# Performance work log

Hardware: AMD Instinct MI355X
Metric: run time of the kernel (lower is better)

## Reference

```python
import jax, jax.numpy as jnp
import numpy as np

B, N, C, K, H, W = 2, 16, 256, 64, 64, 64
NUM_HEADS = 8


def setup_inputs() -> dict:
    key = jax.random.key(0)
    ks = jax.random.split(key, 7)
    return {
        "value": jax.random.normal(ks[0], (B, N, C, H, W), dtype=jnp.float32),
        "key_map": jax.random.normal(ks[1], (B, K, H, W), dtype=jnp.float32),
        "state": jax.random.normal(ks[2], (B, N, K, C), dtype=jnp.float32),
        "b_w": jax.random.normal(ks[3], (NUM_HEADS, C), dtype=jnp.float32) * 0.06,
        "a_w": jax.random.normal(ks[4], (NUM_HEADS, C), dtype=jnp.float32) * 0.06,
        "A_log": jax.random.normal(ks[5], (NUM_HEADS,), dtype=jnp.float32),
        "dt_bias": jax.random.normal(ks[6], (NUM_HEADS,), dtype=jnp.float32),
    }


def reference(value, key_map, state, b_w, a_w, A_log, dt_bias):
    # Gated delta-rule erase-write memory update (state != None branch).
    num_heads = b_w.shape[0]
    rep = value.shape[2] // num_heads  # value_dim // num_heads

    # softmax over key channel dim (stable; matches max-subtract + softmax)
    key_n = jax.nn.softmax(key_map, axis=1)  # [B,K,H,W]

    # v_k = einsum('bkhw, bjhw,bnjv -> bnkv'): fuse via key gram matrix
    # (avoids materializing v_old [B,N,C,H,W])
    gram = jnp.einsum('bkhw,bjhw->bkj', key_n, key_n)      # [B,K,K]
    v_k = jnp.einsum('bkj,bnjv->bnkv', gram, state)        # [B,N,K,C]

    # erase gate beta: sigmoid(state @ b_proj^T), repeat over head groups
    beta = jax.nn.sigmoid(jnp.einsum('bnkc,hc->bnkh', state, b_w))
    beta = jnp.repeat(beta, rep, axis=3)                   # [B,N,K,C]

    # write term
    vk_t = jnp.einsum('bkhw,bnvhw->bnkv', key_n, value)    # [B,N,K,C]

    # decay gate alpha = -exp(A_log) * softplus(state @ a_proj^T + dt_bias)
    alpha = -jnp.exp(A_log) * jax.nn.softplus(
        jnp.einsum('bnkc,hc->bnkh', state, a_w) + dt_bias)
    alpha = jnp.repeat(alpha, rep, axis=3)                 # [B,N,K,C]

    new_state = alpha * (state - beta * v_k) + beta * vk_t  # [B,N,K,C]

    readout = jnp.einsum('bkhw,bnkv->bnvhw', key_n, new_state)  # [B,N,C,H,W]
    return readout
```

## Files before the change

kernel.cpp:

```cpp
#include <hip/hip_runtime.h>
#include <hip/hip_bf16.h>

#define BB 2
#define NN 16
#define CC 256
#define KK 64
#define HW 4096
#define NH 8

typedef __attribute__((ext_vector_type(4))) float f32x4;
typedef __attribute__((ext_vector_type(8))) short s16x8;
typedef __attribute__((ext_vector_type(4))) short s16x4;

__device__ __forceinline__ short f2bf(float f) {
    __hip_bfloat16 h = __float2bfloat16(f);
    return *reinterpret_cast<short*>(&h);
}
__device__ __forceinline__ float bf2f(short s) {
    unsigned int u = ((unsigned int)(unsigned short)s) << 16;
    float f; __builtin_memcpy(&f, &u, 4); return f;
}

__global__ __launch_bounds__(256) void k_pre(const float* __restrict__ state,
                                             const float* __restrict__ b_w,
                                             const float* __restrict__ a_w,
                                             const float* __restrict__ A_log,
                                             const float* __restrict__ dt_bias,
                                             float* __restrict__ betaH,
                                             float* __restrict__ alphaH,
                                             const float* __restrict__ km,
                                             short* __restrict__ kbf,
                                             short* __restrict__ kbfT) {
    __shared__ float red[4][2 * NH];
    const int tid = threadIdx.x;
    const int bid = blockIdx.x;

    if (bid < BB * NN * KK) {
        const int id = bid;
        const int bn = id >> 6;
        const int k = id & 63;
        const float s = state[((size_t)bn * KK + k) * CC + tid];

        float pb[NH], pa[NH];
#pragma unroll
        for (int h = 0; h < NH; h++) {
            pb[h] = s * b_w[h * CC + tid];
            pa[h] = s * a_w[h * CC + tid];
        }
#pragma unroll
        for (int off = 32; off; off >>= 1) {
#pragma unroll
            for (int h = 0; h < NH; h++) {
                pb[h] += __shfl_down(pb[h], off, 64);
                pa[h] += __shfl_down(pa[h], off, 64);
            }
        }
        const int wave = tid >> 6, lane = tid & 63;
        if (lane == 0) {
#pragma unroll
            for (int h = 0; h < NH; h++) { red[wave][h] = pb[h]; red[wave][NH + h] = pa[h]; }
        }
        __syncthreads();
        const int h = tid >> 5;
        float braw = 0.f, araw = 0.f;
#pragma unroll
        for (int w = 0; w < 4; w++) { braw += red[w][h]; araw += red[w][NH + h]; }
        if ((tid & 31) == 0) {
            const float beta = 1.f / (1.f + __expf(-braw));
            const float xx = araw + dt_bias[h];
            const float sp = fmaxf(xx, 0.f) + log1pf(__expf(-fabsf(xx)));
            const float alpha = -__expf(A_log[h]) * sp;
            betaH[(size_t)id * NH + h] = beta;
            alphaH[(size_t)id * NH + h] = alpha;
        }
    } else {
        const int sid = bid - BB * NN * KK;
        const int b = sid >> 5;
        const int w = tid >> 6, lane = tid & 63;
        const int hw = (sid & 31) * 128 + w * 32 + (lane & 31);
        const int half = lane >> 5;
        const float* p = km + ((size_t)b * KK + half * 32) * HW + hw;
        float x[32];
        float m = -1e30f;
#pragma unroll
        for (int k = 0; k < 32; k++) { x[k] = p[(size_t)k * HW]; m = fmaxf(m, x[k]); }
        m = fmaxf(m, __shfl_xor(m, 32, 64));
        float s = 0.f;
#pragma unroll
        for (int k = 0; k < 32; k++) { x[k] = __expf(x[k] - m); s += x[k]; }
        s += __shfl_xor(s, 32, 64);
        const float inv = 1.f / s;
        short* q2 = kbf + ((size_t)b * KK + half * 32) * HW + hw;
#pragma unroll
        for (int k = 0; k < 32; k++) {
            x[k] *= inv;
            q2[(size_t)k * HW] = f2bf(x[k]);
        }
        short* q3 = kbfT + ((size_t)b * HW + hw) * KK + half * 32;
#pragma unroll
        for (int k8 = 0; k8 < 32; k8 += 8) {
            s16x8 v;
#pragma unroll
            for (int j = 0; j < 8; j++) v[j] = f2bf(x[k8 + j]);
            *(s16x8*)(q3 + k8) = v;
        }
    }
}

__global__ __launch_bounds__(256) void k_gram(const short* __restrict__ kbf,
                                              float* __restrict__ gram) {
    const int tid = threadIdx.x;
    const int id = blockIdx.x;
    const int b = (id >= 2080) ? 1 : 0;
    const int t = id - b * 2080;
    int k = (int)((sqrtf(8.f * (float)t + 1.f) - 1.f) * 0.5f);
    while ((k + 1) * (k + 2) / 2 <= t) k++;
    while (k * (k + 1) / 2 > t) k--;
    const int j = t - k * (k + 1) / 2;

    const short* pa = kbf + ((size_t)b * KK + k) * HW + tid * 16;
    const short* pb = kbf + ((size_t)b * KK + j) * HW + tid * 16;
    const s16x8 a0 = *(const s16x8*)pa, a1 = *(const s16x8*)(pa + 8);
    const s16x8 b0 = *(const s16x8*)pb, b1 = *(const s16x8*)(pb + 8);
    float s = 0.f;
#pragma unroll
    for (int i = 0; i < 8; i++) {
        s = fmaf(bf2f(a0[i]), bf2f(b0[i]), s);
        s = fmaf(bf2f(a1[i]), bf2f(b1[i]), s);
    }
#pragma unroll
    for (int off = 32; off; off >>= 1) s += __shfl_down(s, off, 64);
    __shared__ float red[4];
    if ((tid & 63) == 0) red[tid >> 6] = s;
    __syncthreads();
    if (tid == 0) {
        const float tot = red[0] + red[1] + red[2] + red[3];
        gram[((size_t)b * KK + k) * KK + j] = tot;
        gram[((size_t)b * KK + j) * KK + k] = tot;
    }
}

__global__ __launch_bounds__(512) void k_vkt_part(const short* __restrict__ kbf,
                                                  const float* __restrict__ value,
                                                  short* __restrict__ pbuf) {
    const int tid = threadIdx.x;
    const int id = blockIdx.x;
    const int hs = id & 15;
    const int bn = id >> 4;
    const int b  = bn >> 4;
    const int w = tid >> 6, lane = tid & 63;
    const int l15 = lane & 15, hi = lane >> 4;
    const int hw0 = hs * 256;

    __shared__ short Bs[2][256 * 64];
    __shared__ short As[2][64 * 64];

    const int sr = tid >> 3;
    const int sj = tid & 7;
    const float* vbase = value + (size_t)bn * CC * HW + hw0;
    const short* abase = kbf + ((size_t)b * KK + sr) * HW + hw0 + sj * 8;

    f32x4 stgB[2][4][2];
    s16x8 stgA[2];

#define LOADREG(set_, t_)                                                      \
    {                                                                          \
        _Pragma("unroll") for (int i = 0; i < 4; i++) {                        \
            const float* p_ = vbase + (size_t)(sr + i * 64) * HW               \
                              + (t_) * 64 + sj * 8;                            \
            stgB[set_][i][0] = *(const f32x4*)p_;                              \
            stgB[set_][i][1] = *(const f32x4*)(p_ + 4);                        \
        }                                                                      \
        stgA[set_] = *(const s16x8*)(abase + (t_) * 64);                       \
    }
#define WRITE_LDS(set_, buf_)                                                  \
    {                                                                          \
        _Pragma("unroll") for (int i = 0; i < 4; i++) {                        \
            const int r_ = sr + i * 64;                                        \
            s16x8 tv_;                                                         \
            _Pragma("unroll") for (int e = 0; e < 4; e++) {                    \
                tv_[e]     = f2bf(stgB[set_][i][0][e]);                        \
                tv_[4 + e] = f2bf(stgB[set_][i][1][e]);                        \
            }                                                                  \
            *(s16x8*)&Bs[buf_][r_ * 64 + ((sj ^ (r_ & 7)) * 8)] = tv_;         \
        }                                                                      \
        *(s16x8*)&As[buf_][sr * 64 + ((sj ^ (sr & 7)) * 8)] = stgA[set_];      \
    }

    f32x4 acc[2][4];
#pragma unroll
    for (int m2 = 0; m2 < 2; m2++)
#pragma unroll
        for (int n4 = 0; n4 < 4; n4++) acc[m2][n4] = (f32x4){0.f, 0.f, 0.f, 0.f};

    LOADREG(0, 0);
    LOADREG(1, 1);
    WRITE_LDS(0, 0);
    asm volatile("s_waitcnt lgkmcnt(0)" ::: "memory");
    __builtin_amdgcn_s_barrier();

#pragma unroll
    for (int t = 0; t < 4; t++) {
        const int buf = t & 1;
        if (t + 2 < 4) LOADREG(buf, t + 2);
        if (t + 1 < 4) WRITE_LDS((t + 1) & 1, (t + 1) & 1);

        const int swz = l15 & 7;
#pragma unroll
        for (int s = 0; s < 2; s++) {
            s16x8 vfr[2];
#pragma unroll
            for (int m2 = 0; m2 < 2; m2++)
                vfr[m2] = *(const s16x8*)&Bs[buf][(w * 32 + m2 * 16 + l15) * 64 +
                                                 (((s * 4 + hi) ^ swz) * 8)];
#pragma unroll
            for (int n4 = 0; n4 < 4; n4++) {
                const s16x8 afr = *(const s16x8*)&As[buf][(n4 * 16 + l15) * 64 +
                                                          (((s * 4 + hi) ^ swz) * 8)];
                acc[0][n4] = __builtin_amdgcn_mfma_f32_16x16x32_bf16(vfr[0], afr,
                                                                     acc[0][n4], 0, 0, 0);
                acc[1][n4] = __builtin_amdgcn_mfma_f32_16x16x32_bf16(vfr[1], afr,
                                                                     acc[1][n4], 0, 0, 0);
            }
        }
        if (t + 1 < 4) {
            asm volatile("s_waitcnt lgkmcnt(0)" ::: "memory");
            __builtin_amdgcn_s_barrier();
        }
    }
#undef LOADREG
#undef WRITE_LDS

#pragma unroll
    for (int m2 = 0; m2 < 2; m2++)
#pragma unroll
        for (int n4 = 0; n4 < 4; n4++) {
            s16x4 v;
#pragma unroll
            for (int r = 0; r < 4; r++) v[r] = f2bf(acc[m2][n4][r]);
            *(s16x4*)(pbuf + ((((size_t)(id * 8 + w) * 2 + m2) * 4 + n4) * 64
                              + lane) * 4) = v;
        }
}

__global__ __launch_bounds__(256) void k_combine(const short* __restrict__ pbuf,
                                                 const float* __restrict__ gram,
                                                 const float* __restrict__ state,
                                                 const float* __restrict__ betaH,
                                                 const float* __restrict__ alphaH,
                                                 short* __restrict__ nsT) {
    const int tid = threadIdx.x;
    const int id = blockIdx.x;
    const int ct = id & 15;
    const int bn = id >> 4;
    const int b  = bn >> 4;
    const int head = ct >> 1;
    const int wi = ct >> 1, m2 = ct & 1;

    __shared__ float gramL[KK][65];
    __shared__ float stL[KK][17];
    __shared__ float alphaL[KK], betaL[KK];
    __shared__ float nsb[KK][17];

    for (int i = tid; i < KK * KK; i += 256)
        gramL[i >> 6][i & 63] = gram[(size_t)b * KK * KK + i];
    for (int i = tid; i < KK * 16; i += 256)
        stL[i >> 4][i & 15] = state[((size_t)bn * KK + (i >> 4)) * CC + ct * 16 + (i & 15)];
    if (tid < KK) {
        alphaL[tid] = alphaH[((size_t)bn * KK + tid) * NH + head];
        betaL[tid]  = betaH[((size_t)bn * KK + tid) * NH + head];
    }
    __syncthreads();

    const int k = tid >> 2, cq = (tid & 3) * 4;
    const int n4 = k >> 4, l15k = k & 15, hi = tid & 3;

    float vkt[4] = {0.f, 0.f, 0.f, 0.f};
#pragma unroll
    for (int hs = 0; hs < 16; hs++) {
        const int slab = bn * 16 + hs;
        const s16x4 p = *(const s16x4*)(pbuf +
            ((((size_t)(slab * 8 + wi) * 2 + m2) * 4 + n4) * 64 + hi * 16 + l15k) * 4);
#pragma unroll
        for (int i = 0; i < 4; i++) vkt[i] += bf2f(p[i]);
    }

    float vk[4] = {0.f, 0.f, 0.f, 0.f};
#pragma unroll 8
    for (int j = 0; j < KK; j++) {
        const float g = gramL[k][j];
        vk[0] = fmaf(g, stL[j][cq + 0], vk[0]);
        vk[1] = fmaf(g, stL[j][cq + 1], vk[1]);
        vk[2] = fmaf(g, stL[j][cq + 2], vk[2]);
        vk[3] = fmaf(g, stL[j][cq + 3], vk[3]);
    }
    const float al = alphaL[k], be = betaL[k];
#pragma unroll
    for (int i = 0; i < 4; i++)
        nsb[k][cq + i] = al * (stL[k][cq + i] - be * vk[i]) + be * vkt[i];
    __syncthreads();

    const int c = tid >> 4, k4 = (tid & 15) * 4;
    s16x4 v;
#pragma unroll
    for (int i = 0; i < 4; i++) v[i] = f2bf(nsb[k4 + i][c]);
    *(s16x4*)(nsT + ((size_t)bn * CC + ct * 16 + c) * KK + k4) = v;
}

__global__ __launch_bounds__(256) void k_readout_mfma(const short* __restrict__ kbfT,
                                                      const short* __restrict__ nsT,
                                                      float* __restrict__ out) {
    const int tid = threadIdx.x;
    const int id = blockIdx.x;
    const int hwt = id & 63;
    const int bn  = id >> 6;
    const int b   = bn >> 4;
    const int w = tid >> 6, lane = tid & 63;
    const int l15 = lane & 15, hi = lane >> 4;
    const int hw0 = hwt * 64 + w * 16;

    const short* Bp = kbfT + ((size_t)b * HW + hw0 + l15) * KK + hi * 8;
    const s16x8 hwf0 = *(const s16x8*)Bp;
    const s16x8 hwf1 = *(const s16x8*)(Bp + 32);

    const short* Ap = nsT + ((size_t)bn * CC + l15) * KK + hi * 8;
    float* op = out + ((size_t)bn * CC + l15) * HW + hw0 + hi * 4;

#pragma unroll
    for (int ct = 0; ct < 16; ct++) {
        const s16x8 a0 = *(const s16x8*)(Ap + (size_t)(ct * 16) * KK);
        const s16x8 a1 = *(const s16x8*)(Ap + (size_t)(ct * 16) * KK + 32);
        f32x4 acc = (f32x4){0.f, 0.f, 0.f, 0.f};
        acc = __builtin_amdgcn_mfma_f32_16x16x32_bf16(hwf0, a0, acc, 0, 0, 0);
        acc = __builtin_amdgcn_mfma_f32_16x16x32_bf16(hwf1, a1, acc, 0, 0, 0);
        *(f32x4*)(op + (size_t)(ct * 16) * HW) = acc;
    }
}

extern "C" void kernel_launch(void* const* d_in, const int* in_sizes, int n_in,
                              void* d_out, int out_size, void* d_ws, size_t ws_size,
                              hipStream_t stream) {
    const float* value   = (const float*)d_in[0];
    const float* key_map = (const float*)d_in[1];
    const float* state   = (const float*)d_in[2];
    const float* b_w     = (const float*)d_in[3];
    const float* a_w     = (const float*)d_in[4];
    const float* A_log   = (const float*)d_in[5];
    const float* dt_bias = (const float*)d_in[6];
    float* out = (float*)d_out;

    short* kbf   = (short*)d_ws;
    short* kbfT  = kbf + 524288;
    float* gram  = (float*)(kbfT + 524288);
    float* betaH = gram + 8192;
    float* alphaH= betaH + 16384;
    short* nsT   = (short*)(alphaH + 16384);
    short* pbufB = nsT + 524288;

    k_pre<<<BB * NN * KK + BB * (HW / 128), 256, 0, stream>>>(
        state, b_w, a_w, A_log, dt_bias, betaH, alphaH, key_map, kbf, kbfT);
    k_gram<<<BB * (KK * (KK + 1) / 2), 256, 0, stream>>>(kbf, gram);
    k_vkt_part<<<BB * NN * 16, 512, 0, stream>>>(kbf, value, pbufB);
    k_combine<<<BB * NN * 16, 256, 0, stream>>>(pbufB, gram, state, betaH, alphaH, nsT);
    k_readout_mfma<<<BB * NN * (HW / 64), 256, 0, stream>>>(kbfT, nsT, out);
}
```

Baseline: 101.4 us.

## Fuse combine and readout kernels, keeping new-state tile in LDS

Merges the combine kernel (computing the new state tile) with the readout MFMA kernel. Each block now keeps its 16-channel bf16 new-state slice in shared memory and loops over all 64 spatial tiles to write the output, instead of round-tripping nsT through global memory and paying a separate launch. The cost is that readout parallelism drops from 2048 blocks to 512, and each block runs a long serial loop over the spatial tiles. The key map is also re-read by every block.

```diff
diff --git a/kernel.cpp b/kernel.cpp
--- a/kernel.cpp
+++ b/kernel.cpp
@@ -243,12 +243,13 @@
         }
 }
 
-__global__ __launch_bounds__(256) void k_combine(const short* __restrict__ pbuf,
-                                                 const float* __restrict__ gram,
-                                                 const float* __restrict__ state,
-                                                 const float* __restrict__ betaH,
-                                                 const float* __restrict__ alphaH,
-                                                 short* __restrict__ nsT) {
+__global__ __launch_bounds__(256) void k_cr(const short* __restrict__ pbuf,
+                                            const float* __restrict__ gram,
+                                            const float* __restrict__ state,
+                                            const float* __restrict__ betaH,
+                                            const float* __restrict__ alphaH,
+                                            const short* __restrict__ kbfT,
+                                            float* __restrict__ out) {
     const int tid = threadIdx.x;
     const int id = blockIdx.x;
     const int ct = id & 15;
@@ -261,6 +262,7 @@
     __shared__ float stL[KK][17];
     __shared__ float alphaL[KK], betaL[KK];
     __shared__ float nsb[KK][17];
+    __shared__ short nsB[16][72];
 
     for (int i = tid; i < KK * KK; i += 256)
         gramL[i >> 6][i & 63] = gram[(size_t)b * KK * KK + i];
@@ -272,68 +274,64 @@
     }
     __syncthreads();
 
-    const int k = tid >> 2, cq = (tid & 3) * 4;
-    const int n4 = k >> 4, l15k = k & 15, hi = tid & 3;
-
-    float vkt[4] = {0.f, 0.f, 0.f, 0.f};
-#pragma unroll
-    for (int hs = 0; hs < 16; hs++) {
-        const int slab = bn * 16 + hs;
-        const s16x4 p = *(const s16x4*)(pbuf +
-            ((((size_t)(slab * 8 + wi) * 2 + m2) * 4 + n4) * 64 + hi * 16 + l15k) * 4);
-#pragma unroll
-        for (int i = 0; i < 4; i++) vkt[i] += bf2f(p[i]);
-    }
-
-    float vk[4] = {0.f, 0.f, 0.f, 0.f};
+    {
+        const int k = tid >> 2, cq = (tid & 3) * 4;
+        const int n4 = k >> 4, l15k = k & 15, hi4 = tid & 3;
+
+        float vkt[4] = {0.f, 0.f, 0.f, 0.f};
+#pragma unroll
+        for (int hs = 0; hs < 16; hs++) {
+            const int slab = bn * 16 + hs;
+            const s16x4 p = *(const s16x4*)(pbuf +
+                ((((size_t)(slab * 8 + wi) * 2 + m2) * 4 + n4) * 64 + hi4 * 16 + l15k) * 4);
+#pragma unroll
+            for (int i = 0; i < 4; i++) vkt[i] += bf2f(p[i]);
+        }
+
+        float vk[4] = {0.f, 0.f, 0.f, 0.f};
 #pragma unroll 8
-    for (int j = 0; j < KK; j++) {
-        const float g = gramL[k][j];
-        vk[0] = fmaf(g, stL[j][cq + 0], vk[0]);
-        vk[1] = fmaf(g, stL[j][cq + 1], vk[1]);
-        vk[2] = fmaf(g, stL[j][cq + 2], vk[2]);
-        vk[3] = fmaf(g, stL[j][cq + 3], vk[3]);
-    }
-    const float al = alphaL[k], be = betaL[k];
-#pragma unroll
-    for (int i = 0; i < 4; i++)
-        nsb[k][cq + i] = al * (stL[k][cq + i] - be * vk[i]) + be * vkt[i];
+        for (int j = 0; j < KK; j++) {
+            const float g = gramL[k][j];
+            vk[0] = fmaf(g, stL[j][cq + 0], vk[0]);
+            vk[1] = fmaf(g, stL[j][cq + 1], vk[1]);
+            vk[2] = fmaf(g, stL[j][cq + 2], vk[2]);
+            vk[3] = fmaf(g, stL[j][cq + 3], vk[3]);
+        }
+        const float al = alphaL[k], be = betaL[k];
+#pragma unroll
+        for (int i = 0; i < 4; i++)
+            nsb[k][cq + i] = al * (stL[k][cq + i] - be * vk[i]) + be * vkt[i];
+    }
     __syncthreads();
 
-    const int c = tid >> 4, k4 = (tid & 15) * 4;
-    s16x4 v;
-#pragma unroll
-    for (int i = 0; i < 4; i++) v[i] = f2bf(nsb[k4 + i][c]);
-    *(s16x4*)(nsT + ((size_t)bn * CC + ct * 16 + c) * KK + k4) = v;
-}
-
-__global__ __launch_bounds__(256) void k_readout_mfma(const short* __restrict__ kbfT,
-                                                      const short* __restrict__ nsT,
-                                                      float* __restrict__ out) {
-    const int tid = threadIdx.x;
-    const int id = blockIdx.x;
-    const int hwt = id & 63;
-    const int bn  = id >> 6;
-    const int b   = bn >> 4;
+    {
+        const int c = tid >> 4, k4 = (tid & 15) * 4;
+        s16x4 v;
+#pragma unroll
+        for (int i = 0; i < 4; i++) v[i] = f2bf(nsb[k4 + i][c]);
+        *(s16x4*)&nsB[c][k4] = v;
+    }
+    __syncthreads();
+
     const int w = tid >> 6, lane = tid & 63;
     const int l15 = lane & 15, hi = lane >> 4;
-    const int hw0 = hwt * 64 + w * 16;
-
-    const short* Bp = kbfT + ((size_t)b * HW + hw0 + l15) * KK + hi * 8;
-    const s16x8 hwf0 = *(const s16x8*)Bp;
-    const s16x8 hwf1 = *(const s16x8*)(Bp + 32);
-
-    const short* Ap = nsT + ((size_t)bn * CC + l15) * KK + hi * 8;
-    float* op = out + ((size_t)bn * CC + l15) * HW + hw0 + hi * 4;
-
-#pragma unroll
-    for (int ct = 0; ct < 16; ct++) {
-        const s16x8 a0 = *(const s16x8*)(Ap + (size_t)(ct * 16) * KK);
-        const s16x8 a1 = *(const s16x8*)(Ap + (size_t)(ct * 16) * KK + 32);
+
+    const s16x8 cf0 = *(const s16x8*)&nsB[l15][hi * 8];
+    const s16x8 cf1 = *(const s16x8*)&nsB[l15][32 + hi * 8];
+
+    const short* kb = kbfT + ((size_t)b * HW + l15) * KK + hi * 8;
+    float* ob = out + ((size_t)bn * CC + ct * 16 + l15) * HW + hi * 4;
+
+#pragma unroll 4
+    for (int mt = 0; mt < 64; mt++) {
+        const int hw0 = mt * 64 + w * 16;
+        const short* Bp = kb + (size_t)hw0 * KK;
+        const s16x8 hwf0 = *(const s16x8*)Bp;
+        const s16x8 hwf1 = *(const s16x8*)(Bp + 32);
         f32x4 acc = (f32x4){0.f, 0.f, 0.f, 0.f};
-        acc = __builtin_amdgcn_mfma_f32_16x16x32_bf16(hwf0, a0, acc, 0, 0, 0);
-        acc = __builtin_amdgcn_mfma_f32_16x16x32_bf16(hwf1, a1, acc, 0, 0, 0);
-        *(f32x4*)(op + (size_t)(ct * 16) * HW) = acc;
+        acc = __builtin_amdgcn_mfma_f32_16x16x32_bf16(hwf0, cf0, acc, 0, 0, 0);
+        acc = __builtin_amdgcn_mfma_f32_16x16x32_bf16(hwf1, cf1, acc, 0, 0, 0);
+        *(f32x4*)(ob + hw0) = acc;
     }
 }
 
@@ -354,13 +352,12 @@
     float* gram  = (float*)(kbfT + 524288);
     float* betaH = gram + 8192;
     float* alphaH= betaH + 16384;
-    short* nsT   = (short*)(alphaH + 16384);
-    short* pbufB = nsT + 524288;
+    short* pbufB = (short*)(alphaH + 16384);
 
     k_pre<<<BB * NN * KK + BB * (HW / 128), 256, 0, stream>>>(
         state, b_w, a_w, A_log, dt_bias, betaH, alphaH, key_map, kbf, kbfT);
     k_gram<<<BB * (KK * (KK + 1) / 2), 256, 0, stream>>>(kbf, gram);
     k_vkt_part<<<BB * NN * 16, 512, 0, stream>>>(kbf, value, pbufB);
-    k_combine<<<BB * NN * 16, 256, 0, stream>>>(pbufB, gram, state, betaH, alphaH, nsT);
-    k_readout_mfma<<<BB * NN * (HW / 64), 256, 0, stream>>>(kbfT, nsT, out);
-}
+    k_cr<<<BB * NN * 16, 256, 0, stream>>>(pbufB, gram, state, betaH, alphaH,
+                                           kbfT, out);
+}
```

Result: faster. 97.33 us (-4.0%).
